# Optimization experiments

Measured on AMD Instinct MI355X. Metric: run time of the kernel, lower is better.

## Reference

```python
import jax, jax.numpy as jnp
import numpy as np

B, S, H, D = 2, 2048, 16, 64


def setup_inputs() -> dict:
    key0 = jax.random.key(0)
    kq, kk = jax.random.split(key0)
    query = jax.random.normal(kq, (B, S, H, D), dtype=jnp.float32)
    key = jax.random.normal(kk, (B, S, H, D), dtype=jnp.float32)
    # causal mask, broadcastable to [B, H, q, k]
    mask = jnp.tril(jnp.ones((S, S), dtype=bool))[None, None, :, :]
    mask = jnp.broadcast_to(mask, (B, 1, S, S))
    return {"query": query, "key": key, "mask": mask}


def reference(query, key, mask):
    dtype = query.dtype
    qk_features = query.shape[-1]
    q = query / jnp.sqrt(qk_features).astype(dtype)
    # [B, H, q, k]
    attn_weights = jnp.einsum('...qhd,...khd->...hqk', q, key)
    big_neg = jnp.finfo(dtype).min
    attn_weights = jnp.where(mask, attn_weights, big_neg)
    attn_weights = jax.nn.softmax(attn_weights).astype(dtype)
    return attn_weights
```

## Files before the change

### kernel.cpp

```cpp
#include <hip/hip_runtime.h>
#include <stdint.h>
#include <stddef.h>

#define B_ 2
#define H_ 16
#define S_ 2048
#define D_ 64

#define TQ 32
#define TK 256
#define NW 4
#define BLK (NW*64)
#define NQT (S_/TQ)
#define NBLK_F (B_*H_*NQT)
#define NBLK_S (32*36)
#define NBLK_W (32*8*4)

typedef __attribute__((ext_vector_type(8))) short bf16x8;
typedef __attribute__((ext_vector_type(4))) float f32x4;

__device__ __forceinline__ unsigned short f2bf(float f) {
  union { float f; uint32_t u; } v; v.f = f;
  uint32_t r = v.u + 0x7FFFu + ((v.u >> 16) & 1u);
  return (unsigned short)(r >> 16);
}

__device__ __forceinline__ void stage_k(const f32x4* kp, unsigned short* ldsK,
                                        int b, int h, int kc, int tid) {
#pragma unroll
  for (int i = 0; i < 8; ++i) {
    const int g  = i * BLK + tid;
    const int kl = g >> 3;
    const int gd = g & 7;
    const size_t gb = (((size_t)b * S_ + (kc * TK + kl)) * H_ + h) * (D_ / 4) + gd * 2;
    f32x4 v0 = kp[gb];
    f32x4 v1 = kp[gb + 1];
    bf16x8 bv;
    bv[0] = (short)f2bf(v0.x); bv[1] = (short)f2bf(v0.y);
    bv[2] = (short)f2bf(v0.z); bv[3] = (short)f2bf(v0.w);
    bv[4] = (short)f2bf(v1.x); bv[5] = (short)f2bf(v1.y);
    bv[6] = (short)f2bf(v1.z); bv[7] = (short)f2bf(v1.w);
    const int idx = (kl * D_ + gd * 8) ^ ((kl & 7) << 3);
    *reinterpret_cast<bf16x8*>(&ldsK[idx]) = bv;
  }
}

__device__ __forceinline__ void stage_q(const f32x4* qp, unsigned short (*ldsQ)[72],
                                        int b, int h, int qb, int tid) {
#pragma unroll
  for (int i = 0; i < 2; ++i) {
    const int g   = i * BLK + tid;
    const int row = g >> 4;
    const int d4  = g & 15;
    f32x4 v = qp[(((size_t)b * S_ + (qb + row)) * H_ + h) * (D_ / 4) + d4];
    unsigned short* dst = &ldsQ[row][d4 * 4];
    dst[0] = f2bf(v.x * 0.125f);
    dst[1] = f2bf(v.y * 0.125f);
    dst[2] = f2bf(v.z * 0.125f);
    dst[3] = f2bf(v.w * 0.125f);
  }
}

__device__ __forceinline__ void mfma_tile(const unsigned short* ldsK,
                                          const bf16x8 qfr[2][2],
                                          f32x4 acc[4][2], int w, int colk, int rg) {
#pragma unroll
  for (int kf = 0; kf < 4; ++kf) {
    const int krow = w * 64 + kf * 16 + colk;
    const int i0 = (krow * D_ + rg * 8) ^ ((krow & 7) << 3);
    const int i1 = (krow * D_ + 32 + rg * 8) ^ ((krow & 7) << 3);
    bf16x8 a0 = *reinterpret_cast<const bf16x8*>(&ldsK[i0]);
    bf16x8 a1 = *reinterpret_cast<const bf16x8*>(&ldsK[i1]);
#pragma unroll
    for (int qf = 0; qf < 2; ++qf) {
      acc[kf][qf] = __builtin_amdgcn_mfma_f32_16x16x32_bf16(a0, qfr[qf][0], acc[kf][qf], 0, 0, 0);
      acc[kf][qf] = __builtin_amdgcn_mfma_f32_16x16x32_bf16(a1, qfr[qf][1], acc[kf][qf], 0, 0, 0);
    }
  }
}

__device__ __forceinline__ void load_qfr(const unsigned short (*ldsQ)[72],
                                         bf16x8 qfr[2][2], int colk, int rg) {
#pragma unroll
  for (int qf = 0; qf < 2; ++qf)
#pragma unroll
    for (int hh = 0; hh < 2; ++hh)
      qfr[qf][hh] = *reinterpret_cast<const bf16x8*>(&ldsQ[qf * 16 + colk][hh * 32 + rg * 8]);
}

__global__ __launch_bounds__(BLK, 4)
void attn_sums_v4(const float* __restrict__ Qg, const float* __restrict__ Kg,
                  float* __restrict__ wsPart) {
  __shared__ unsigned short ldsK[TK * D_];
  __shared__ unsigned short ldsQ[TQ][72];
  __shared__ float ldsSum[NW][2][16];

  const int tid  = threadIdx.x;
  const int lane = tid & 63;
  const int w    = tid >> 6;
  const int colk = lane & 15;
  const int rg   = lane >> 4;

  int bid = (int)blockIdx.x;
  bid = (bid & 7) * (NBLK_S / 8) + (bid >> 3);
  const int bh = bid / 36;
  int j = bid - bh * 36;
  int kc = 0, base = 0;
  while (j >= base + (8 - kc)) { base += 8 - kc; ++kc; }
  const int ci = j - base;
  const int qt0 = kc * 8 + ci * 8;
  const int b = bh >> 4, h = bh & (H_ - 1);

  const f32x4* qp = reinterpret_cast<const f32x4*>(Qg);
  const f32x4* kp = reinterpret_cast<const f32x4*>(Kg);

  stage_k(kp, ldsK, b, h, kc, tid);

  for (int i = 0; i < 8; ++i) {
    const int qt = qt0 + i;
    const int qb = qt * TQ;
    __syncthreads();
    stage_q(qp, ldsQ, b, h, qb, tid);
    __syncthreads();
    bf16x8 qfr[2][2];
    load_qfr(ldsQ, qfr, colk, rg);
    f32x4 acc[4][2];
#pragma unroll
    for (int kf = 0; kf < 4; ++kf)
#pragma unroll
      for (int qf = 0; qf < 2; ++qf) acc[kf][qf] = (f32x4)0.0f;
    mfma_tile(ldsK, qfr, acc, w, colk, rg);

    float rsum[2] = {0.f, 0.f};
#pragma unroll
    for (int kf = 0; kf < 4; ++kf)
#pragma unroll
      for (int qf = 0; qf < 2; ++qf)
#pragma unroll
        for (int r = 0; r < 4; ++r) {
          const int kk = kc * TK + w * 64 + kf * 16 + rg * 4 + r;
          const int qq = qb + qf * 16 + colk;
          rsum[qf] += (kk <= qq) ? __expf(acc[kf][qf][r]) : 0.f;
        }
#pragma unroll
    for (int qf = 0; qf < 2; ++qf) {
      float v = rsum[qf];
      v += __shfl_xor(v, 16);
      v += __shfl_xor(v, 32);
      rsum[qf] = v;
    }
    if (rg == 0) { ldsSum[w][0][colk] = rsum[0]; ldsSum[w][1][colk] = rsum[1]; }
    __syncthreads();
    if (tid < 32) {
      const int qf = tid >> 4, ck = tid & 15;
      const float s = ldsSum[0][qf][ck] + ldsSum[1][qf][ck] +
                      ldsSum[2][qf][ck] + ldsSum[3][qf][ck];
      wsPart[((size_t)bh * 8 + kc) * S_ + qb + tid] = s;
    }
  }
}

__global__ __launch_bounds__(BLK, 4)
void attn_store_v4(const float* __restrict__ Qg, const float* __restrict__ Kg,
                   const float* __restrict__ wsPart, float* __restrict__ Og) {
  __shared__ unsigned short ldsK[TK * D_];
  __shared__ unsigned short ldsQ[TQ][72];
  __shared__ float rinvL[512];

  const int tid  = threadIdx.x;
  const int lane = tid & 63;
  const int w    = tid >> 6;
  const int colk = lane & 15;
  const int rg   = lane >> 4;

  int bid = (int)blockIdx.x;
  bid = (bid & 7) * (NBLK_W / 8) + (bid >> 3);
  const int bh = bid >> 5;
  const int r5 = bid & 31;
  const int kc = r5 >> 2;
  const int qg = r5 & 3;
  const int b = bh >> 4, h = bh & (H_ - 1);
  const int kmin = kc * TK;
  const int row0 = qg * 512;

  if (kmin > row0 + 511) {
    const int rr = tid >> 3, cg = tid & 7;
    f32x4 z = {0.f, 0.f, 0.f, 0.f};
#pragma unroll
    for (int tr = 0; tr < 16; ++tr) {
      float* rp = Og + ((size_t)bh * S_ + row0 + tr * 32 + rr) * S_ + kmin;
#pragma unroll
      for (int c = 0; c < 8; ++c)
        __builtin_nontemporal_store(z, reinterpret_cast<f32x4*>(rp + (c * 8 + cg) * 4));
    }
    return;
  }

  const f32x4* qp = reinterpret_cast<const f32x4*>(Qg);
  const f32x4* kp = reinterpret_cast<const f32x4*>(Kg);

  stage_k(kp, ldsK, b, h, kc, tid);

  for (int lr = tid; lr < 512; lr += BLK) {
    const int q = row0 + lr;
    if (q >= kmin) {
      float s = 0.f;
      const int top = q >> 8;
      for (int c2 = 0; c2 <= top; ++c2)
        s += wsPart[((size_t)bh * 8 + c2) * S_ + q];
      rinvL[lr] = 1.0f / s;
    }
  }

  bool synced = false;
  for (int i = 0; i < 16; ++i) {
    const int qt = qg * 16 + i;
    const int qb = qt * TQ;
    float* outT = Og + ((size_t)bh * S_ + qb) * S_ + kmin;

    if (kmin > qb + 31) {
      const int rr = tid >> 3, cg = tid & 7;
      f32x4 z = {0.f, 0.f, 0.f, 0.f};
      float* rp = outT + (size_t)rr * S_;
#pragma unroll
      for (int c = 0; c < 8; ++c)
        __builtin_nontemporal_store(z, reinterpret_cast<f32x4*>(rp + (c * 8 + cg) * 4));
      continue;
    }

    __syncthreads();
    (void)synced;
    stage_q(qp, ldsQ, b, h, qb, tid);
    __syncthreads();
    bf16x8 qfr[2][2];
    load_qfr(ldsQ, qfr, colk, rg);
    f32x4 acc[4][2];
#pragma unroll
    for (int kf = 0; kf < 4; ++kf)
#pragma unroll
      for (int qf = 0; qf < 2; ++qf) acc[kf][qf] = (f32x4)0.0f;
    mfma_tile(ldsK, qfr, acc, w, colk, rg);

#pragma unroll
    for (int kf = 0; kf < 4; ++kf)
#pragma unroll
      for (int qf = 0; qf < 2; ++qf) {
        const int qq = qb + qf * 16 + colk;
        const float ri = rinvL[i * 32 + qf * 16 + colk];
        f32x4 o;
#pragma unroll
        for (int r = 0; r < 4; ++r) {
          const int kk = kmin + w * 64 + kf * 16 + rg * 4 + r;
          o[r] = (kk <= qq) ? __expf(acc[kf][qf][r]) * ri : 0.f;
        }
        __builtin_nontemporal_store(o, reinterpret_cast<f32x4*>(
            outT + (size_t)(qf * 16 + colk) * S_ + w * 64 + kf * 16 + rg * 4));
      }
  }
}

__global__ __launch_bounds__(BLK, 4)
void attn_weights_fused(const float* __restrict__ Qg, const float* __restrict__ Kg,
                        float* __restrict__ Og) {
  __shared__ unsigned short ldsK[TK * D_];
  __shared__ unsigned short ldsQ[TQ][72];
  __shared__ float ldsSum[NW][2][16];

  const int tid  = threadIdx.x;
  const int lane = tid & 63;
  const int w    = tid >> 6;
  const int colk = lane & 15;
  const int rg   = lane >> 4;

  int bid = (int)blockIdx.x;
  bid = (bid & 7) * (NBLK_F / 8) + (bid >> 3);
  const int qt = bid & (NQT - 1);
  const int bh = bid >> 6;
  const int h  = bh & (H_ - 1);
  const int b  = bh >> 4;
  const int qb = qt * TQ;
  const int tmax = qb >> 8;

  float* outp = Og + ((size_t)bh * S_ + qb) * S_;
  {
    const int row = tid >> 3;
    f32x4 z = {0.f, 0.f, 0.f, 0.f};
    float* rp = outp + (size_t)row * S_;
    for (int c = (tmax + 1) * (TK / 4) + (tid & 7); c < S_ / 4; c += 8)
      *reinterpret_cast<f32x4*>(rp + c * 4) = z;
  }
  const f32x4* qp = reinterpret_cast<const f32x4*>(Qg);
  const f32x4* kp = reinterpret_cast<const f32x4*>(Kg);
  stage_q(qp, ldsQ, b, h, qb, tid);
  __syncthreads();
  bf16x8 qfr[2][2];
  load_qfr(ldsQ, qfr, colk, rg);
  float rsum[2] = {0.f, 0.f};
  for (int t = 0; t <= tmax; ++t) {
    stage_k(kp, ldsK, b, h, t, tid);
    __syncthreads();
    f32x4 acc[4][2];
#pragma unroll
    for (int kf = 0; kf < 4; ++kf)
#pragma unroll
      for (int qf = 0; qf < 2; ++qf) acc[kf][qf] = (f32x4)0.0f;
    mfma_tile(ldsK, qfr, acc, w, colk, rg);
#pragma unroll
    for (int kf = 0; kf < 4; ++kf)
#pragma unroll
      for (int qf = 0; qf < 2; ++qf)
#pragma unroll
        for (int r = 0; r < 4; ++r) {
          const int kk = t * TK + w * 64 + kf * 16 + rg * 4 + r;
          const int qq = qb + qf * 16 + colk;
          rsum[qf] += (kk <= qq) ? __expf(acc[kf][qf][r]) : 0.f;
        }
    __syncthreads();
  }
#pragma unroll
  for (int qf = 0; qf < 2; ++qf) {
    float v = rsum[qf];
    v += __shfl_xor(v, 16);
    v += __shfl_xor(v, 32);
    rsum[qf] = v;
  }
  if (rg == 0) { ldsSum[w][0][colk] = rsum[0]; ldsSum[w][1][colk] = rsum[1]; }
  __syncthreads();
  float rinv[2];
#pragma unroll
  for (int qf = 0; qf < 2; ++qf)
    rinv[qf] = 1.0f / (ldsSum[0][qf][colk] + ldsSum[1][qf][colk] +
                       ldsSum[2][qf][colk] + ldsSum[3][qf][colk]);
  for (int t = 0; t <= tmax; ++t) {
    stage_k(kp, ldsK, b, h, t, tid);
    __syncthreads();
    f32x4 acc[4][2];
#pragma unroll
    for (int kf = 0; kf < 4; ++kf)
#pragma unroll
      for (int qf = 0; qf < 2; ++qf) acc[kf][qf] = (f32x4)0.0f;
    mfma_tile(ldsK, qfr, acc, w, colk, rg);
#pragma unroll
    for (int kf = 0; kf < 4; ++kf)
#pragma unroll
      for (int qf = 0; qf < 2; ++qf) {
        f32x4 o;
#pragma unroll
        for (int r = 0; r < 4; ++r) {
          const int kk = t * TK + w * 64 + kf * 16 + rg * 4 + r;
          const int qq = qb + qf * 16 + colk;
          o[r] = (kk <= qq) ? __expf(acc[kf][qf][r]) * rinv[qf] : 0.f;
        }
        *reinterpret_cast<f32x4*>(outp + (size_t)(qf * 16 + colk) * S_ +
                                  t * TK + w * 64 + kf * 16 + rg * 4) = o;
      }
    __syncthreads();
  }
}

extern "C" void kernel_launch(void* const* d_in, const int* in_sizes, int n_in,
                              void* d_out, int out_size, void* d_ws, size_t ws_size,
                              hipStream_t stream) {
  const float* Qg = (const float*)d_in[0];
  const float* Kg = (const float*)d_in[1];
  float* Og = (float*)d_out;
  const size_t need = (size_t)32 * 8 * S_ * sizeof(float);
  if (ws_size >= need) {
    float* wsPart = (float*)d_ws;
    attn_sums_v4 <<<dim3(NBLK_S), dim3(BLK), 0, stream>>>(Qg, Kg, wsPart);
    attn_store_v4<<<dim3(NBLK_W), dim3(BLK), 0, stream>>>(Qg, Kg, wsPart, Og);
  } else {
    attn_weights_fused<<<dim3(NBLK_F), dim3(BLK), 0, stream>>>(Qg, Kg, Og);
  }
}
```

Measured before the change: 161.6 us.

## Prefetch next Q tile into registers and skip fully masked tiles upfront

The store kernel now loads the next Q tile from global memory into registers while the current tile is computed. It writes that tile to LDS after the fragments are read, using raw s_barrier calls in place of the two __syncthreads per iteration. Fully masked leading Q tiles are zero-filled in one coalesced sweep before the loop, and the loop starts at the first unmasked tile. The zero-fill loops are rewritten so each warp writes contiguous 1KB row segments. This adds register pressure and relies on hand-placed waitcnt and barriers being correct for the single-buffered ldsQ.

```diff
diff --git a/kernel.cpp b/kernel.cpp
--- a/kernel.cpp
+++ b/kernel.cpp
@@ -61,6 +61,43 @@
   }
 }
 
+struct QPre { f32x4 a, b; };
+__device__ __forceinline__ QPre qpre_load(const f32x4* qp, int b, int h, int qb, int tid) {
+  QPre r;
+  {
+    const int g = tid;
+    r.a = qp[(((size_t)b * S_ + (qb + (g >> 4))) * H_ + h) * (D_ / 4) + (g & 15)];
+  }
+  {
+    const int g = BLK + tid;
+    r.b = qp[(((size_t)b * S_ + (qb + (g >> 4))) * H_ + h) * (D_ / 4) + (g & 15)];
+  }
+  return r;
+}
+__device__ __forceinline__ void qpre_write(unsigned short (*ldsQ)[72], const QPre& p, int tid) {
+#pragma unroll
+  for (int i = 0; i < 2; ++i) {
+    const int g   = i * BLK + tid;
+    const int row = g >> 4;
+    const int d4  = g & 15;
+    const f32x4 v = i ? p.b : p.a;
+    unsigned short* dst = &ldsQ[row][d4 * 4];
+    dst[0] = f2bf(v.x * 0.125f);
+    dst[1] = f2bf(v.y * 0.125f);
+    dst[2] = f2bf(v.z * 0.125f);
+    dst[3] = f2bf(v.w * 0.125f);
+  }
+}
+
+__device__ __forceinline__ void load_qfr(const unsigned short (*ldsQ)[72],
+                                         bf16x8 qfr[2][2], int colk, int rg) {
+#pragma unroll
+  for (int qf = 0; qf < 2; ++qf)
+#pragma unroll
+    for (int hh = 0; hh < 2; ++hh)
+      qfr[qf][hh] = *reinterpret_cast<const bf16x8*>(&ldsQ[qf * 16 + colk][hh * 32 + rg * 8]);
+}
+
 __device__ __forceinline__ void mfma_tile(const unsigned short* ldsK,
                                           const bf16x8 qfr[2][2],
                                           f32x4 acc[4][2], int w, int colk, int rg) {
@@ -77,15 +114,6 @@
       acc[kf][qf] = __builtin_amdgcn_mfma_f32_16x16x32_bf16(a1, qfr[qf][1], acc[kf][qf], 0, 0, 0);
     }
   }
-}
-
-__device__ __forceinline__ void load_qfr(const unsigned short (*ldsQ)[72],
-                                         bf16x8 qfr[2][2], int colk, int rg) {
-#pragma unroll
-  for (int qf = 0; qf < 2; ++qf)
-#pragma unroll
-    for (int hh = 0; hh < 2; ++hh)
-      qfr[qf][hh] = *reinterpret_cast<const bf16x8*>(&ldsQ[qf * 16 + colk][hh * 32 + rg * 8]);
 }
 
 __global__ __launch_bounds__(BLK, 4)
@@ -161,7 +189,7 @@
 }
 
 __global__ __launch_bounds__(BLK, 4)
-void attn_store_v4(const float* __restrict__ Qg, const float* __restrict__ Kg,
+void attn_store_v6(const float* __restrict__ Qg, const float* __restrict__ Kg,
                    const float* __restrict__ wsPart, float* __restrict__ Og) {
   __shared__ unsigned short ldsK[TK * D_];
   __shared__ unsigned short ldsQ[TQ][72];
@@ -184,20 +212,34 @@
   const int row0 = qg * 512;
 
   if (kmin > row0 + 511) {
-    const int rr = tid >> 3, cg = tid & 7;
     f32x4 z = {0.f, 0.f, 0.f, 0.f};
-#pragma unroll
-    for (int tr = 0; tr < 16; ++tr) {
-      float* rp = Og + ((size_t)bh * S_ + row0 + tr * 32 + rr) * S_ + kmin;
-#pragma unroll
-      for (int c = 0; c < 8; ++c)
-        __builtin_nontemporal_store(z, reinterpret_cast<f32x4*>(rp + (c * 8 + cg) * 4));
+#pragma unroll 4
+    for (int it = 0; it < 128; ++it) {
+      const int g = it * BLK + tid;
+      const int row = row0 + (g >> 6);
+      const int cg = g & 63;
+      __builtin_nontemporal_store(z, reinterpret_cast<f32x4*>(
+          Og + ((size_t)bh * S_ + row) * S_ + kmin + cg * 4));
     }
     return;
   }
 
   const f32x4* qp = reinterpret_cast<const f32x4*>(Qg);
   const f32x4* kp = reinterpret_cast<const f32x4*>(Kg);
+
+  const int i0 = (kmin > row0) ? ((kmin - row0) >> 5) : 0;
+
+  if (i0 > 0) {
+    f32x4 z = {0.f, 0.f, 0.f, 0.f};
+#pragma unroll 4
+    for (int it = 0; it < 64; ++it) {
+      const int g = it * BLK + tid;
+      const int row = row0 + (g >> 6);
+      const int cg = g & 63;
+      __builtin_nontemporal_store(z, reinterpret_cast<f32x4*>(
+          Og + ((size_t)bh * S_ + row) * S_ + kmin + cg * 4));
+    }
+  }
 
   stage_k(kp, ldsK, b, h, kc, tid);
 
@@ -212,28 +254,29 @@
     }
   }
 
-  bool synced = false;
-  for (int i = 0; i < 16; ++i) {
-    const int qt = qg * 16 + i;
-    const int qb = qt * TQ;
+  stage_q(qp, ldsQ, b, h, row0 + i0 * TQ, tid);
+  __syncthreads();
+
+  QPre pre;
+  if (i0 + 1 < 16) pre = qpre_load(qp, b, h, row0 + (i0 + 1) * TQ, tid);
+
+  for (int i = i0; i < 16; ++i) {
+    const int qb = row0 + i * TQ;
     float* outT = Og + ((size_t)bh * S_ + qb) * S_ + kmin;
 
-    if (kmin > qb + 31) {
-      const int rr = tid >> 3, cg = tid & 7;
-      f32x4 z = {0.f, 0.f, 0.f, 0.f};
-      float* rp = outT + (size_t)rr * S_;
-#pragma unroll
-      for (int c = 0; c < 8; ++c)
-        __builtin_nontemporal_store(z, reinterpret_cast<f32x4*>(rp + (c * 8 + cg) * 4));
-      continue;
-    }
-
-    __syncthreads();
-    (void)synced;
-    stage_q(qp, ldsQ, b, h, qb, tid);
-    __syncthreads();
     bf16x8 qfr[2][2];
     load_qfr(ldsQ, qfr, colk, rg);
+    asm volatile("s_waitcnt lgkmcnt(0)" ::: "memory");
+    __builtin_amdgcn_sched_barrier(0);
+    __builtin_amdgcn_s_barrier();
+
+    if (i + 1 < 16) {
+      qpre_write(ldsQ, pre, tid);
+      if (i + 2 < 16) pre = qpre_load(qp, b, h, row0 + (i + 2) * TQ, tid);
+      asm volatile("s_waitcnt lgkmcnt(0)" ::: "memory");
+    }
+    __builtin_amdgcn_s_barrier();
+
     f32x4 acc[4][2];
 #pragma unroll
     for (int kf = 0; kf < 4; ++kf)
@@ -368,7 +411,7 @@
   if (ws_size >= need) {
     float* wsPart = (float*)d_ws;
     attn_sums_v4 <<<dim3(NBLK_S), dim3(BLK), 0, stream>>>(Qg, Kg, wsPart);
-    attn_store_v4<<<dim3(NBLK_W), dim3(BLK), 0, stream>>>(Qg, Kg, wsPart, Og);
+    attn_store_v6<<<dim3(NBLK_W), dim3(BLK), 0, stream>>>(Qg, Kg, wsPart, Og);
   } else {
     attn_weights_fused<<<dim3(NBLK_F), dim3(BLK), 0, stream>>>(Qg, Kg, Og);
   }
```

Result: faster. 154.4 us (median of 3 runs) (-4.5%).
